# Kernel optimization log

Measured on AMD Instinct MI355X. Metric: run time of the kernel, lower is better.

Reference implementation:

```python
import jax, jax.numpy as jnp
import numpy as np

EMBED_DIM = 1024
NUM_HEADS = 16
HEAD_DIM = EMBED_DIM // NUM_HEADS  # 64
GRID_H, GRID_W = 24, 24
BASE = 10000.0


def rope2d_cache(head_dim=HEAD_DIM, grid_h=GRID_H, grid_w=GRID_W, base=BASE):
    # "Concatenated Embeddings" 2D RoPE cache -> (cos, sin), each [grid_h*grid_w, head_dim]
    pos_dim = head_dim // 2
    inv_freq = 1.0 / (base ** (jnp.arange(0, pos_dim, 2, dtype=jnp.float32) / pos_dim))
    max_grid = max(grid_h, grid_w)
    positions = jnp.arange(max_grid, dtype=jnp.float32)
    freqs = positions[:, None] * inv_freq[None, :]            # [max_grid, pos_dim//2]
    emb_1d = jnp.concatenate([freqs, freqs], axis=-1)          # [max_grid, pos_dim]
    h_emb = jnp.broadcast_to(emb_1d[:grid_h, None, :], (grid_h, grid_w, pos_dim))
    w_emb = jnp.broadcast_to(emb_1d[None, :grid_w, :], (grid_h, grid_w, pos_dim))
    emb_2d = jnp.concatenate([h_emb, w_emb], axis=-1).reshape(-1, head_dim)
    return jnp.cos(emb_2d), jnp.sin(emb_2d)


def rotate_half(x):
    x1, x2 = jnp.split(x, 2, axis=-1)
    return jnp.concatenate([-x2, x1], axis=-1)


def setup_inputs() -> dict:
    key = jax.random.key(0)
    ks = jax.random.split(key, 9)
    B, S, E = 16, GRID_H * GRID_W + 1, EMBED_DIM
    s = 1.0 / np.sqrt(E)
    inp = {
        "hidden_states": jax.random.normal(ks[0], (B, S, E), dtype=jnp.float32),
        "Wq": jax.random.normal(ks[1], (E, E), dtype=jnp.float32) * s,
        "bq": jnp.zeros((E,), dtype=jnp.float32),
        "Wk": jax.random.normal(ks[2], (E, E), dtype=jnp.float32) * s,
        "bk": jnp.zeros((E,), dtype=jnp.float32),
        "Wv": jax.random.normal(ks[3], (E, E), dtype=jnp.float32) * s,
        "bv": jnp.zeros((E,), dtype=jnp.float32),
        "Wo": jax.random.normal(ks[4], (E, E), dtype=jnp.float32) * s,
        "bo": jnp.zeros((E,), dtype=jnp.float32),
    }
    return inp


def reference(hidden_states, Wq, bq, Wk, bk, Wv, bv, Wo, bo):
    B, S, E = hidden_states.shape
    H, D = NUM_HEADS, HEAD_DIM
    scale = D ** -0.5

    def proj(W, b):
        # torch Linear: x @ W.T + b; reshape to [B, H, S, D]
        y = jnp.einsum('bse,fe->bsf', hidden_states, W) + b
        return y.reshape(B, S, H, D).transpose(0, 2, 1, 3)

    q = proj(Wq, bq)
    k = proj(Wk, bk)
    v = proj(Wv, bv)

    cos, sin = rope2d_cache()                 # [num_patches, D]
    cos = cos[None, None, :, :]
    sin = sin[None, None, :, :]

    # CLS token at position 0 is untouched; RoPE applied to patch tokens 1:
    qp = q[:, :, 1:, :]
    kp = k[:, :, 1:, :]
    qp = qp * cos + rotate_half(qp) * sin
    kp = kp * cos + rotate_half(kp) * sin
    q = jnp.concatenate([q[:, :, :1, :], qp], axis=2)
    k = jnp.concatenate([k[:, :, :1, :], kp], axis=2)

    scores = jnp.einsum('bhqd,bhkd->bhqk', q, k) * scale   # [B,H,S,S]
    attn = jax.nn.softmax(scores, axis=-1)
    out = jnp.einsum('bhqk,bhkd->bhqd', attn, v)           # [B,H,S,D]
    out = out.transpose(0, 2, 1, 3).reshape(B, S, E)
    out = jnp.einsum('bse,fe->bsf', out, Wo) + bo
    return out
```

## Files before the change

kernel.cpp:

```cpp
#include <hip/hip_runtime.h>
#include <hip/hip_bf16.h>
#include <stdint.h>

typedef __bf16 bf16_t;
typedef __attribute__((ext_vector_type(4))) float floatx4;
typedef __attribute__((ext_vector_type(8))) __bf16 bf16x8;
typedef __attribute__((ext_vector_type(4))) __bf16 bf16x4;

#define MFMA16(a, b, c) __builtin_amdgcn_mfma_f32_16x16x32_bf16(a, b, c, 0, 0, 0)

#define GLOAD_LDS16(gsrc, ldst)                                                          \
  __builtin_amdgcn_global_load_lds((const __attribute__((address_space(1))) void*)(gsrc),\
                                   (__attribute__((address_space(3))) void*)(ldst),      \
                                   16, 0, 0)

#define BATCH 16
#define SEQ   577
#define EMB   1024
#define NH    16
#define HD    64
#define SPAD  640
#define MROWS (BATCH * SEQ)
#define MPAD  9344

#define EXP_C 0.1803368801111404f

#define OFF_H  0ULL
#define OFF_WQ 19136512ULL
#define OFF_WK 21233664ULL
#define OFF_WV 23330816ULL
#define OFF_WO 25427968ULL
#define OFF_Q  27525120ULL
#define OFF_K  48496640ULL
#define OFF_VT 69468160ULL
#define OFF_AO 90439680ULL

__global__ __launch_bounds__(256) void k_cast(
    const float4* __restrict__ hs, const float4* __restrict__ wq,
    const float4* __restrict__ wk, const float4* __restrict__ wv,
    const float4* __restrict__ wo, bf16x4* __restrict__ hb, bf16x4* __restrict__ wqb,
    bf16x4* __restrict__ wkb, bf16x4* __restrict__ wvb, bf16x4* __restrict__ wob) {
  int idx = blockIdx.x * 256 + threadIdx.x;
  const int H4 = MROWS * EMB / 4;
  const int W4 = EMB * EMB / 4;
  const float4* src;
  bf16x4* dst;
  int i;
  if (idx < H4) {
    src = hs; dst = hb; i = idx;
  } else {
    int r = idx - H4;
    int w = r / W4;
    if (w >= 4) return;
    i = r - w * W4;
    src = (w == 0) ? wq : (w == 1) ? wk : (w == 2) ? wv : wo;
    dst = (w == 0) ? wqb : (w == 1) ? wkb : (w == 2) ? wvb : wob;
  }
  float4 v = src[i];
  bf16x4 o;
  o.x = (bf16_t)v.x; o.y = (bf16_t)v.y; o.z = (bf16_t)v.z; o.w = (bf16_t)v.w;
  dst[i] = o;
}

__device__ __forceinline__ void gemm_core_128(const bf16_t* __restrict__ A,
                                              const bf16_t* __restrict__ W, int m0, int n0,
                                              bf16_t* As, bf16_t* Bs, floatx4 acc[4][4]) {
  const int t = threadIdx.x;
  const int wid = t >> 6;
  const int lane = t & 63;
  const int quad = lane >> 4;
  const int c = lane & 15;
  const int wr = wid >> 1;
  const int wc = wid & 1;

#pragma unroll
  for (int i = 0; i < 4; i++)
#pragma unroll
    for (int j = 0; j < 4; j++) {
      floatx4 z = {0.f, 0.f, 0.f, 0.f};
      acc[i][j] = z;
    }

  for (int k0 = 0; k0 < EMB; k0 += 32) {
    __syncthreads();
#pragma unroll
    for (int i = 0; i < 2; i++) {
      int ci = i * 256 + t;
      int row = ci >> 2, off = (ci & 3) * 8;
      const bf16_t* ga = A + (size_t)(m0 + row) * EMB + k0 + off;
      GLOAD_LDS16(ga, (char*)As + (i * 256 + wid * 64) * 16);
      const bf16_t* gb = W + (size_t)(n0 + row) * EMB + k0 + off;
      GLOAD_LDS16(gb, (char*)Bs + (i * 256 + wid * 64) * 16);
    }
    __syncthreads();
    bf16x8 af[4], bfr[4];
#pragma unroll
    for (int mi = 0; mi < 4; mi++)
      af[mi] = *(const bf16x8*)(As + (wr * 64 + mi * 16 + c) * 32 + quad * 8);
#pragma unroll
    for (int ni = 0; ni < 4; ni++)
      bfr[ni] = *(const bf16x8*)(Bs + (wc * 64 + ni * 16 + c) * 32 + quad * 8);
#pragma unroll
    for (int mi = 0; mi < 4; mi++)
#pragma unroll
      for (int ni = 0; ni < 4; ni++) acc[mi][ni] = MFMA16(af[mi], bfr[ni], acc[mi][ni]);
  }
}

__global__ __launch_bounds__(256) void k_qkv(const bf16_t* __restrict__ A,
                                             const bf16_t* __restrict__ Wq,
                                             const bf16_t* __restrict__ Wk,
                                             const bf16_t* __restrict__ Wv,
                                             const float* __restrict__ bq,
                                             const float* __restrict__ bk,
                                             const float* __restrict__ bv,
                                             bf16_t* __restrict__ qb, bf16_t* __restrict__ kb,
                                             bf16_t* __restrict__ vtb) {
  __shared__ bf16_t As[128 * 32];
  __shared__ bf16_t Bs[128 * 32];
  const int z = blockIdx.z;
  const bf16_t* W = (z == 0) ? Wq : (z == 1) ? Wk : Wv;
  const float* bias = (z == 0) ? bq : (z == 1) ? bk : bv;
  const int m0 = blockIdx.x * 128;
  const int n0 = blockIdx.y * 128;
  floatx4 acc[4][4];
  gemm_core_128(A, W, m0, n0, As, Bs, acc);

  const int t = threadIdx.x;
  const int wid = t >> 6, lane = t & 63, quad = lane >> 4, c = lane & 15;
  const int wr = wid >> 1, wc = wid & 1;
  const int hh = blockIdx.y * 2 + wc;
  float bias_v[4];
#pragma unroll
  for (int ni = 0; ni < 4; ni++) bias_v[ni] = bias[n0 + wc * 64 + ni * 16 + c];

  const float invf = exp2f(-(float)c * 0.8304820237218405f);

#pragma unroll
  for (int mi = 0; mi < 4; mi++) {
#pragma unroll
    for (int r = 0; r < 4; r++) {
      int m = m0 + wr * 64 + mi * 16 + quad * 4 + r;
      if (m >= MROWS) continue;
      int bb = m / SEQ;
      int s = m - bb * SEQ;
      if (z < 2) {
        float ch = 1.f, sh = 0.f, cw = 1.f, sw = 0.f;
        if (s > 0) {
          int p = s - 1;
          int hp = p / 24, wp = p - (p / 24) * 24;
          __sincosf((float)hp * invf, &sh, &ch);
          __sincosf((float)wp * invf, &sw, &cw);
        }
        bf16_t* dst = (z == 0) ? qb : kb;
        size_t rowoff = ((size_t)(bb * NH + hh) * SPAD + s) * HD;
#pragma unroll
        for (int ni = 0; ni < 4; ni++) {
          float val = acc[mi][ni][r] + bias_v[ni];
          float part = acc[mi][ni ^ 2][r] + bias_v[ni ^ 2];
          float rot = (ni < 2) ? -part : part;
          float cs = (ni < 2) ? ch : cw;
          float sn = (ni < 2) ? sh : sw;
          dst[rowoff + ni * 16 + c] = (bf16_t)(val * cs + rot * sn);
        }
      } else {
        size_t base = (size_t)(bb * NH + hh) * HD;
#pragma unroll
        for (int ni = 0; ni < 4; ni++) {
          float val = acc[mi][ni][r] + bias_v[ni];
          int d = ni * 16 + c;
          vtb[(base + d) * SPAD + s] = (bf16_t)val;
        }
      }
    }
  }
}

#define PSTR 72
__global__ __launch_bounds__(256) void k_attn(const bf16_t* __restrict__ qb,
                                              const bf16_t* __restrict__ kb,
                                              const bf16_t* __restrict__ vtb,
                                              bf16_t* __restrict__ ao) {
  __shared__ bf16_t Qs[128 * 64];
  __shared__ bf16_t Ks[64 * PSTR];
  __shared__ bf16_t Vs[64 * PSTR];
  __shared__ bf16_t Ps[4 * 32 * PSTR];
  const int t = threadIdx.x, wid = t >> 6, lane = t & 63, quad = lane >> 4, c = lane & 15;
  const int qt = blockIdx.x, hh = blockIdx.y, bb = blockIdx.z;
  const size_t bh = (size_t)bb * NH + hh;
  const bf16_t* qbase = qb + bh * SPAD * HD + (size_t)qt * 128 * HD;
  const bf16_t* kbase = kb + bh * SPAD * HD;
  const bf16_t* vbase = vtb + bh * HD * SPAD;

#pragma unroll
  for (int i = 0; i < 4; i++) {
    int ci = i * 256 + t;
    *(uint4*)(Qs + ci * 8) = *(const uint4*)(qbase + ci * 8);
  }

  uint4 kr[2], vr[2];
#pragma unroll
  for (int j = 0; j < 2; j++) {
    int ci = j * 256 + t;
    int row = ci >> 3, off = (ci & 7) * 8;
    kr[j] = *(const uint4*)(kbase + (size_t)row * HD + off);
    vr[j] = *(const uint4*)(vbase + (size_t)row * SPAD + off);
  }
  __syncthreads();

  bf16x8 aq[2][2];
#pragma unroll
  for (int mi = 0; mi < 2; mi++)
#pragma unroll
    for (int h = 0; h < 2; h++)
      aq[mi][h] = *(const bf16x8*)(Qs + (wid * 32 + mi * 16 + c) * 64 + h * 32 + quad * 8);

  bf16x8 ones;
#pragma unroll
  for (int i = 0; i < 8; i++) ones[i] = (bf16_t)1.0f;

  floatx4 acc_o[2][4], acc_l[2];
#pragma unroll
  for (int mi = 0; mi < 2; mi++) {
    floatx4 z = {0.f, 0.f, 0.f, 0.f};
    acc_l[mi] = z;
#pragma unroll
    for (int nd = 0; nd < 4; nd++) acc_o[mi][nd] = z;
  }

  bf16_t* Pw = Ps + wid * 32 * PSTR;

  for (int kt = 0; kt < 10; kt++) {
    __syncthreads();
#pragma unroll
    for (int j = 0; j < 2; j++) {
      int ci = j * 256 + t;
      int row = ci >> 3, off = (ci & 7) * 8;
      *(uint4*)((char*)Ks + (row * PSTR + off) * 2) = kr[j];
      *(uint4*)((char*)Vs + (row * PSTR + off) * 2) = vr[j];
    }
    __syncthreads();
    if (kt < 9) {
#pragma unroll
      for (int j = 0; j < 2; j++) {
        int ci = j * 256 + t;
        int row = ci >> 3, off = (ci & 7) * 8;
        kr[j] = *(const uint4*)(kbase + (size_t)((kt + 1) * 64 + row) * HD + off);
        vr[j] = *(const uint4*)(vbase + (size_t)row * SPAD + (kt + 1) * 64 + off);
      }
    }

    floatx4 sc[2][4];
#pragma unroll
    for (int ni = 0; ni < 4; ni++) {
      bf16x8 k0 = *(const bf16x8*)(Ks + (ni * 16 + c) * PSTR + quad * 8);
      bf16x8 k1 = *(const bf16x8*)(Ks + (ni * 16 + c) * PSTR + 32 + quad * 8);
#pragma unroll
      for (int mi = 0; mi < 2; mi++) {
        floatx4 zz = {0.f, 0.f, 0.f, 0.f};
        zz = MFMA16(aq[mi][0], k0, zz);
        zz = MFMA16(aq[mi][1], k1, zz);
        sc[mi][ni] = zz;
      }
    }
    if (kt == 9) {
#pragma unroll
      for (int ni = 0; ni < 4; ni++)
        if (ni * 16 + c >= 1)
#pragma unroll
          for (int mi = 0; mi < 2; mi++)
#pragma unroll
            for (int r = 0; r < 4; r++) sc[mi][ni][r] = -1e30f;
    }
#pragma unroll
    for (int mi = 0; mi < 2; mi++)
#pragma unroll
      for (int ni = 0; ni < 4; ni++)
#pragma unroll
        for (int r = 0; r < 4; r++) {
          float p = exp2f(sc[mi][ni][r] * EXP_C);
          Pw[(mi * 16 + quad * 4 + r) * PSTR + ni * 16 + c] = (bf16_t)p;
        }
    bf16x8 pa[2][2];
#pragma unroll
    for (int mi = 0; mi < 2; mi++)
#pragma unroll
      for (int h = 0; h < 2; h++)
        pa[mi][h] = *(const bf16x8*)(Pw + (mi * 16 + c) * PSTR + h * 32 + quad * 8);
#pragma unroll
    for (int nd = 0; nd < 4; nd++) {
      bf16x8 v0 = *(const bf16x8*)(Vs + (nd * 16 + c) * PSTR + quad * 8);
      bf16x8 v1 = *(const bf16x8*)(Vs + (nd * 16 + c) * PSTR + 32 + quad * 8);
#pragma unroll
      for (int mi = 0; mi < 2; mi++) {
        acc_o[mi][nd] = MFMA16(pa[mi][0], v0, acc_o[mi][nd]);
        acc_o[mi][nd] = MFMA16(pa[mi][1], v1, acc_o[mi][nd]);
      }
    }
#pragma unroll
    for (int mi = 0; mi < 2; mi++) {
      acc_l[mi] = MFMA16(pa[mi][0], ones, acc_l[mi]);
      acc_l[mi] = MFMA16(pa[mi][1], ones, acc_l[mi]);
    }
  }

#pragma unroll
  for (int mi = 0; mi < 2; mi++)
#pragma unroll
    for (int r = 0; r < 4; r++) {
      int q = qt * 128 + wid * 32 + mi * 16 + quad * 4 + r;
      if (q < SEQ) {
        size_t mrow = (size_t)bb * SEQ + q;
        float inv_l = 1.f / acc_l[mi][r];
#pragma unroll
        for (int nd = 0; nd < 4; nd++)
          ao[mrow * EMB + hh * HD + nd * 16 + c] = (bf16_t)(acc_o[mi][nd][r] * inv_l);
      }
    }
}

__global__ __launch_bounds__(256) void k_oproj(const bf16_t* __restrict__ A,
                                               const bf16_t* __restrict__ Wo,
                                               const float* __restrict__ bo,
                                               float* __restrict__ out) {
  __shared__ bf16_t As[128 * 32];
  __shared__ bf16_t Bs[128 * 32];
  const int m0 = blockIdx.x * 128, n0 = blockIdx.y * 128;
  floatx4 acc[4][4];
  gemm_core_128(A, Wo, m0, n0, As, Bs, acc);
  const int t = threadIdx.x, wid = t >> 6, lane = t & 63, quad = lane >> 4, c = lane & 15;
  const int wr = wid >> 1, wc = wid & 1;
  float bias_v[4];
#pragma unroll
  for (int ni = 0; ni < 4; ni++) bias_v[ni] = bo[n0 + wc * 64 + ni * 16 + c];
#pragma unroll
  for (int mi = 0; mi < 4; mi++)
#pragma unroll
    for (int r = 0; r < 4; r++) {
      int m = m0 + wr * 64 + mi * 16 + quad * 4 + r;
      if (m >= MROWS) continue;
#pragma unroll
      for (int ni = 0; ni < 4; ni++)
        out[(size_t)m * EMB + n0 + wc * 64 + ni * 16 + c] = acc[mi][ni][r] + bias_v[ni];
    }
}

extern "C" void kernel_launch(void* const* d_in, const int* in_sizes, int n_in, void* d_out,
                              int out_size, void* d_ws, size_t ws_size, hipStream_t stream) {
  const float* hs = (const float*)d_in[0];
  const float* Wq = (const float*)d_in[1];
  const float* bq = (const float*)d_in[2];
  const float* Wk = (const float*)d_in[3];
  const float* bk = (const float*)d_in[4];
  const float* Wv = (const float*)d_in[5];
  const float* bv = (const float*)d_in[6];
  const float* Wo = (const float*)d_in[7];
  const float* bo = (const float*)d_in[8];
  float* out = (float*)d_out;
  char* ws = (char*)d_ws;

  bf16_t* hb = (bf16_t*)(ws + OFF_H);
  bf16_t* wqb = (bf16_t*)(ws + OFF_WQ);
  bf16_t* wkb = (bf16_t*)(ws + OFF_WK);
  bf16_t* wvb = (bf16_t*)(ws + OFF_WV);
  bf16_t* wob = (bf16_t*)(ws + OFF_WO);
  bf16_t* qbuf = (bf16_t*)(ws + OFF_Q);
  bf16_t* kbuf = (bf16_t*)(ws + OFF_K);
  bf16_t* vtbuf = (bf16_t*)(ws + OFF_VT);
  bf16_t* aob = (bf16_t*)(ws + OFF_AO);


  k_cast<<<13328, 256, 0, stream>>>((const float4*)hs, (const float4*)Wq, (const float4*)Wk,
                                    (const float4*)Wv, (const float4*)Wo, (bf16x4*)hb,
                                    (bf16x4*)wqb, (bf16x4*)wkb, (bf16x4*)wvb, (bf16x4*)wob);

  dim3 gq(73, 8, 3);
  k_qkv<<<gq, 256, 0, stream>>>(hb, wqb, wkb, wvb, bq, bk, bv, qbuf, kbuf, vtbuf);

  dim3 ga(5, 16, 16);
  k_attn<<<ga, 256, 0, stream>>>(qbuf, kbuf, vtbuf, aob);

  dim3 go(73, 8, 1);
  k_oproj<<<go, 256, 0, stream>>>(aob, wob, bo, out);
}
```

Before: 362.4 us.

## Fuse Q/K/V projections into one block sharing the A tile

Each QKV block now computes all three projections for one 128x128 output tile, loading the hidden-state tile once into LDS and reusing it across Wq, Wk and Wv. This cuts A-tile global traffic and launches a third as many blocks. Both GEMM grids are also reordered so that blockIdx.x walks the N dimension, which lets neighbouring blocks share A rows in cache. The cost is 192 accumulator floats per thread and more LDS per block, which may lower occupancy or cause register spills.

New measurement: 403.6 us. 1.11x slower.

```diff
diff --git a/kernel.cpp b/kernel.cpp
--- a/kernel.cpp
+++ b/kernel.cpp
@@ -62,51 +62,6 @@
   dst[i] = o;
 }
 
-__device__ __forceinline__ void gemm_core_128(const bf16_t* __restrict__ A,
-                                              const bf16_t* __restrict__ W, int m0, int n0,
-                                              bf16_t* As, bf16_t* Bs, floatx4 acc[4][4]) {
-  const int t = threadIdx.x;
-  const int wid = t >> 6;
-  const int lane = t & 63;
-  const int quad = lane >> 4;
-  const int c = lane & 15;
-  const int wr = wid >> 1;
-  const int wc = wid & 1;
-
-#pragma unroll
-  for (int i = 0; i < 4; i++)
-#pragma unroll
-    for (int j = 0; j < 4; j++) {
-      floatx4 z = {0.f, 0.f, 0.f, 0.f};
-      acc[i][j] = z;
-    }
-
-  for (int k0 = 0; k0 < EMB; k0 += 32) {
-    __syncthreads();
-#pragma unroll
-    for (int i = 0; i < 2; i++) {
-      int ci = i * 256 + t;
-      int row = ci >> 2, off = (ci & 3) * 8;
-      const bf16_t* ga = A + (size_t)(m0 + row) * EMB + k0 + off;
-      GLOAD_LDS16(ga, (char*)As + (i * 256 + wid * 64) * 16);
-      const bf16_t* gb = W + (size_t)(n0 + row) * EMB + k0 + off;
-      GLOAD_LDS16(gb, (char*)Bs + (i * 256 + wid * 64) * 16);
-    }
-    __syncthreads();
-    bf16x8 af[4], bfr[4];
-#pragma unroll
-    for (int mi = 0; mi < 4; mi++)
-      af[mi] = *(const bf16x8*)(As + (wr * 64 + mi * 16 + c) * 32 + quad * 8);
-#pragma unroll
-    for (int ni = 0; ni < 4; ni++)
-      bfr[ni] = *(const bf16x8*)(Bs + (wc * 64 + ni * 16 + c) * 32 + quad * 8);
-#pragma unroll
-    for (int mi = 0; mi < 4; mi++)
-#pragma unroll
-      for (int ni = 0; ni < 4; ni++) acc[mi][ni] = MFMA16(af[mi], bfr[ni], acc[mi][ni]);
-  }
-}
-
 __global__ __launch_bounds__(256) void k_qkv(const bf16_t* __restrict__ A,
                                              const bf16_t* __restrict__ Wq,
                                              const bf16_t* __restrict__ Wk,
@@ -117,59 +72,99 @@
                                              bf16_t* __restrict__ qb, bf16_t* __restrict__ kb,
                                              bf16_t* __restrict__ vtb) {
   __shared__ bf16_t As[128 * 32];
-  __shared__ bf16_t Bs[128 * 32];
-  const int z = blockIdx.z;
-  const bf16_t* W = (z == 0) ? Wq : (z == 1) ? Wk : Wv;
-  const float* bias = (z == 0) ? bq : (z == 1) ? bk : bv;
-  const int m0 = blockIdx.x * 128;
-  const int n0 = blockIdx.y * 128;
-  floatx4 acc[4][4];
-  gemm_core_128(A, W, m0, n0, As, Bs, acc);
-
+  __shared__ bf16_t Bs[3 * 128 * 32];
+  const int n0 = blockIdx.x * 128;
+  const int m0 = blockIdx.y * 128;
   const int t = threadIdx.x;
   const int wid = t >> 6, lane = t & 63, quad = lane >> 4, c = lane & 15;
   const int wr = wid >> 1, wc = wid & 1;
-  const int hh = blockIdx.y * 2 + wc;
-  float bias_v[4];
-#pragma unroll
-  for (int ni = 0; ni < 4; ni++) bias_v[ni] = bias[n0 + wc * 64 + ni * 16 + c];
-
+
+  floatx4 acc[3][4][4];
+#pragma unroll
+  for (int z = 0; z < 3; z++)
+#pragma unroll
+    for (int i = 0; i < 4; i++)
+#pragma unroll
+      for (int j = 0; j < 4; j++) {
+        floatx4 zz = {0.f, 0.f, 0.f, 0.f};
+        acc[z][i][j] = zz;
+      }
+
+  for (int k0 = 0; k0 < EMB; k0 += 32) {
+    __syncthreads();
+#pragma unroll
+    for (int i = 0; i < 2; i++) {
+      int ci = i * 256 + t;
+      int row = ci >> 2, off = (ci & 3) * 8;
+      GLOAD_LDS16(A + (size_t)(m0 + row) * EMB + k0 + off, (char*)As + (i * 256 + wid * 64) * 16);
+      GLOAD_LDS16(Wq + (size_t)(n0 + row) * EMB + k0 + off,
+                  (char*)Bs + (i * 256 + wid * 64) * 16);
+      GLOAD_LDS16(Wk + (size_t)(n0 + row) * EMB + k0 + off,
+                  (char*)Bs + 8192 + (i * 256 + wid * 64) * 16);
+      GLOAD_LDS16(Wv + (size_t)(n0 + row) * EMB + k0 + off,
+                  (char*)Bs + 16384 + (i * 256 + wid * 64) * 16);
+    }
+    __syncthreads();
+    bf16x8 af[4];
+#pragma unroll
+    for (int mi = 0; mi < 4; mi++)
+      af[mi] = *(const bf16x8*)(As + (wr * 64 + mi * 16 + c) * 32 + quad * 8);
+#pragma unroll
+    for (int z = 0; z < 3; z++) {
+      bf16x8 bfr[4];
+#pragma unroll
+      for (int ni = 0; ni < 4; ni++)
+        bfr[ni] = *(const bf16x8*)(Bs + z * 4096 + (wc * 64 + ni * 16 + c) * 32 + quad * 8);
+#pragma unroll
+      for (int mi = 0; mi < 4; mi++)
+#pragma unroll
+        for (int ni = 0; ni < 4; ni++) acc[z][mi][ni] = MFMA16(af[mi], bfr[ni], acc[z][mi][ni]);
+    }
+  }
+
+  const int hh = blockIdx.x * 2 + wc;
   const float invf = exp2f(-(float)c * 0.8304820237218405f);
 
-#pragma unroll
-  for (int mi = 0; mi < 4; mi++) {
-#pragma unroll
-    for (int r = 0; r < 4; r++) {
-      int m = m0 + wr * 64 + mi * 16 + quad * 4 + r;
-      if (m >= MROWS) continue;
-      int bb = m / SEQ;
-      int s = m - bb * SEQ;
-      if (z < 2) {
-        float ch = 1.f, sh = 0.f, cw = 1.f, sw = 0.f;
-        if (s > 0) {
-          int p = s - 1;
-          int hp = p / 24, wp = p - (p / 24) * 24;
-          __sincosf((float)hp * invf, &sh, &ch);
-          __sincosf((float)wp * invf, &sw, &cw);
-        }
-        bf16_t* dst = (z == 0) ? qb : kb;
-        size_t rowoff = ((size_t)(bb * NH + hh) * SPAD + s) * HD;
-#pragma unroll
-        for (int ni = 0; ni < 4; ni++) {
-          float val = acc[mi][ni][r] + bias_v[ni];
-          float part = acc[mi][ni ^ 2][r] + bias_v[ni ^ 2];
-          float rot = (ni < 2) ? -part : part;
-          float cs = (ni < 2) ? ch : cw;
-          float sn = (ni < 2) ? sh : sw;
-          dst[rowoff + ni * 16 + c] = (bf16_t)(val * cs + rot * sn);
-        }
-      } else {
-        size_t base = (size_t)(bb * NH + hh) * HD;
-#pragma unroll
-        for (int ni = 0; ni < 4; ni++) {
-          float val = acc[mi][ni][r] + bias_v[ni];
-          int d = ni * 16 + c;
-          vtb[(base + d) * SPAD + s] = (bf16_t)val;
+  for (int z = 0; z < 3; z++) {
+    const float* bias = (z == 0) ? bq : (z == 1) ? bk : bv;
+    float bias_v[4];
+#pragma unroll
+    for (int ni = 0; ni < 4; ni++) bias_v[ni] = bias[n0 + wc * 64 + ni * 16 + c];
+#pragma unroll
+    for (int mi = 0; mi < 4; mi++) {
+#pragma unroll
+      for (int r = 0; r < 4; r++) {
+        int m = m0 + wr * 64 + mi * 16 + quad * 4 + r;
+        if (m >= MROWS) continue;
+        int bb = m / SEQ;
+        int s = m - bb * SEQ;
+        if (z < 2) {
+          float ch = 1.f, sh = 0.f, cw = 1.f, sw = 0.f;
+          if (s > 0) {
+            int p = s - 1;
+            int hp = p / 24, wp = p - (p / 24) * 24;
+            __sincosf((float)hp * invf, &sh, &ch);
+            __sincosf((float)wp * invf, &sw, &cw);
+          }
+          bf16_t* dst = (z == 0) ? qb : kb;
+          size_t rowoff = ((size_t)(bb * NH + hh) * SPAD + s) * HD;
+#pragma unroll
+          for (int ni = 0; ni < 4; ni++) {
+            float val = acc[z][mi][ni][r] + bias_v[ni];
+            float part = acc[z][mi][ni ^ 2][r] + bias_v[ni ^ 2];
+            float rot = (ni < 2) ? -part : part;
+            float cs = (ni < 2) ? ch : cw;
+            float sn = (ni < 2) ? sh : sw;
+            dst[rowoff + ni * 16 + c] = (bf16_t)(val * cs + rot * sn);
+          }
+        } else {
+          size_t base = (size_t)(bb * NH + hh) * HD;
+#pragma unroll
+          for (int ni = 0; ni < 4; ni++) {
+            float val = acc[z][mi][ni][r] + bias_v[ni];
+            int d = ni * 16 + c;
+            vtb[(base + d) * SPAD + s] = (bf16_t)val;
+          }
         }
       }
     }
@@ -325,11 +320,40 @@
                                                float* __restrict__ out) {
   __shared__ bf16_t As[128 * 32];
   __shared__ bf16_t Bs[128 * 32];
-  const int m0 = blockIdx.x * 128, n0 = blockIdx.y * 128;
+  const int n0 = blockIdx.x * 128, m0 = blockIdx.y * 128;
+  const int t = threadIdx.x;
+  const int wid = t >> 6, lane = t & 63, quad = lane >> 4, c = lane & 15;
+  const int wr = wid >> 1, wc = wid & 1;
   floatx4 acc[4][4];
-  gemm_core_128(A, Wo, m0, n0, As, Bs, acc);
-  const int t = threadIdx.x, wid = t >> 6, lane = t & 63, quad = lane >> 4, c = lane & 15;
-  const int wr = wid >> 1, wc = wid & 1;
+#pragma unroll
+  for (int i = 0; i < 4; i++)
+#pragma unroll
+    for (int j = 0; j < 4; j++) {
+      floatx4 z = {0.f, 0.f, 0.f, 0.f};
+      acc[i][j] = z;
+    }
+  for (int k0 = 0; k0 < EMB; k0 += 32) {
+    __syncthreads();
+#pragma unroll
+    for (int i = 0; i < 2; i++) {
+      int ci = i * 256 + t;
+      int row = ci >> 2, off = (ci & 3) * 8;
+      GLOAD_LDS16(A + (size_t)(m0 + row) * EMB + k0 + off, (char*)As + (i * 256 + wid * 64) * 16);
+      GLOAD_LDS16(Wo + (size_t)(n0 + row) * EMB + k0 + off, (char*)Bs + (i * 256 + wid * 64) * 16);
+    }
+    __syncthreads();
+    bf16x8 af[4], bfr[4];
+#pragma unroll
+    for (int mi = 0; mi < 4; mi++)
+      af[mi] = *(const bf16x8*)(As + (wr * 64 + mi * 16 + c) * 32 + quad * 8);
+#pragma unroll
+    for (int ni = 0; ni < 4; ni++)
+      bfr[ni] = *(const bf16x8*)(Bs + (wc * 64 + ni * 16 + c) * 32 + quad * 8);
+#pragma unroll
+    for (int mi = 0; mi < 4; mi++)
+#pragma unroll
+      for (int ni = 0; ni < 4; ni++) acc[mi][ni] = MFMA16(af[mi], bfr[ni], acc[mi][ni]);
+  }
   float bias_v[4];
 #pragma unroll
   for (int ni = 0; ni < 4; ni++) bias_v[ni] = bo[n0 + wc * 64 + ni * 16 + c];
@@ -374,12 +398,12 @@
                                     (const float4*)Wv, (const float4*)Wo, (bf16x4*)hb,
                                     (bf16x4*)wqb, (bf16x4*)wkb, (bf16x4*)wvb, (bf16x4*)wob);
 
-  dim3 gq(73, 8, 3);
+  dim3 gq(8, 73);
   k_qkv<<<gq, 256, 0, stream>>>(hb, wqb, wkb, wvb, bq, bk, bv, qbuf, kbuf, vtbuf);
 
   dim3 ga(5, 16, 16);
   k_attn<<<ga, 256, 0, stream>>>(qbuf, kbuf, vtbuf, aob);
 
-  dim3 go(73, 8, 1);
+  dim3 go(8, 73);
   k_oproj<<<go, 256, 0, stream>>>(aob, wob, bo, out);
 }
```
